# Performance work log

Measured on AMD Instinct MI355X. Metric: run time of the kernel, lower is better.

Reference implementation:

```python
import jax, jax.numpy as jnp
import numpy as np

D_MODEL = 1024
D_FF = 4096
NUM_EXPERTS = 8
TOP_K = 2


def setup_inputs() -> dict:
    key = jax.random.key(0)
    ks = jax.random.split(key, 10)
    s = 0.02
    x = jax.random.normal(ks[0], (2, 1024, D_MODEL), dtype=jnp.float32)
    # router gate (nn.Linear(d_model, num_experts))
    Wr = jax.random.normal(ks[1], (D_MODEL, NUM_EXPERTS), dtype=jnp.float32) * s
    br = jnp.zeros((NUM_EXPERTS,), dtype=jnp.float32)
    # stacked expert weights
    Wg = jax.random.normal(ks[2], (NUM_EXPERTS, D_MODEL, D_FF), dtype=jnp.float32) * s
    bg = jnp.zeros((NUM_EXPERTS, D_FF), dtype=jnp.float32)
    Wu = jax.random.normal(ks[3], (NUM_EXPERTS, D_MODEL, D_FF), dtype=jnp.float32) * s
    bu = jnp.zeros((NUM_EXPERTS, D_FF), dtype=jnp.float32)
    Wd = jax.random.normal(ks[4], (NUM_EXPERTS, D_FF, D_MODEL), dtype=jnp.float32) * s
    bd = jnp.zeros((NUM_EXPERTS, D_MODEL), dtype=jnp.float32)
    return {"x": x, "Wr": Wr, "br": br, "Wg": Wg, "bg": bg,
            "Wu": Wu, "bu": bu, "Wd": Wd, "bd": bd}


def reference(x, Wr, br, Wg, bg, Wu, bu, Wd, bd):
    B, S, D = x.shape
    E = Wg.shape[0]
    xt = x.reshape(-1, D)                       # [T, d]
    T = xt.shape[0]
    # router: softmax in float32, top-k, renormalize (Mixtral-style)
    logits = xt @ Wr + br                       # [T, E]
    probs = jax.nn.softmax(logits.astype(jnp.float32), axis=-1)
    rw, sel = jax.lax.top_k(probs, TOP_K)       # [T, K]
    rw = rw / jnp.sum(rw, axis=-1, keepdims=True)
    # per-token per-expert combine weight (0 if expert not selected)
    w_full = jnp.zeros((T, E), dtype=rw.dtype).at[
        jnp.arange(T)[:, None], sel].add(rw)    # [T, E]
    # SwiGLU experts, computed densely over all tokens then masked-combined
    g = jnp.einsum('td,edf->etf', xt, Wg) + bg[:, None, :]   # [E, T, f]
    u = jnp.einsum('td,edf->etf', xt, Wu) + bu[:, None, :]
    h = jax.nn.silu(g) * u
    y = jnp.einsum('etf,efd->etd', h, Wd) + bd[:, None, :]    # [E, T, d]
    out = jnp.einsum('te,etd->td', w_full.astype(x.dtype), y)
    return out.reshape(B, S, D)
```

## Files before the change

### kernel.cpp

```cpp
#include <hip/hip_runtime.h>

typedef float floatx4 __attribute__((ext_vector_type(4)));
typedef __bf16 bf16x4 __attribute__((ext_vector_type(4)));
typedef __bf16 bf16x8 __attribute__((ext_vector_type(8)));

#define D_MODEL 1024
#define D_FF 4096
#define NE 8

__device__ __forceinline__ int lds_off(int row, int k) {
    return row * 32 + ((((k >> 3) ^ ((row >> 2) & 3)) << 3) | (k & 7));
}

__global__ __launch_bounds__(256) void router_kernel(
    const float* __restrict__ x, const float* __restrict__ Wr,
    const float* __restrict__ br, int* __restrict__ cnt,
    int* __restrict__ list, float* __restrict__ w_slot, int T)
{
    int wv = threadIdx.x >> 6;
    int lane = threadIdx.x & 63;
    int t = blockIdx.x * 4 + wv;
    if (t >= T) return;

    const float* xp = x + (size_t)t * D_MODEL;
    float acc[8] = {0.f,0.f,0.f,0.f,0.f,0.f,0.f,0.f};
#pragma unroll
    for (int i = 0; i < 16; ++i) {
        int d = i * 64 + lane;
        float xv = xp[d];
        float4 w0 = *(const float4*)(Wr + d * 8);
        float4 w1 = *(const float4*)(Wr + d * 8 + 4);
        acc[0] += xv * w0.x; acc[1] += xv * w0.y;
        acc[2] += xv * w0.z; acc[3] += xv * w0.w;
        acc[4] += xv * w1.x; acc[5] += xv * w1.y;
        acc[6] += xv * w1.z; acc[7] += xv * w1.w;
    }
#pragma unroll
    for (int off = 32; off >= 1; off >>= 1) {
#pragma unroll
        for (int e = 0; e < 8; ++e)
            acc[e] += __shfl_down(acc[e], off, 64);
    }
    if (lane == 0) {
        float l[8];
#pragma unroll
        for (int e = 0; e < 8; ++e) l[e] = acc[e] + br[e];
        int i0 = 0; float v0 = l[0];
#pragma unroll
        for (int e = 1; e < 8; ++e) if (l[e] > v0) { v0 = l[e]; i0 = e; }
        int i1 = -1; float v1 = -3.4e38f;
#pragma unroll
        for (int e = 0; e < 8; ++e) if (e != i0 && l[e] > v1) { v1 = l[e]; i1 = e; }
        float ex = __expf(v1 - v0);
        float w0 = 1.f / (1.f + ex);
        float w1 = ex / (1.f + ex);
        int p0 = atomicAdd(&cnt[i0], 1);
        list[i0 * T + p0] = 2 * t;
        int p1 = atomicAdd(&cnt[i1], 1);
        list[i1 * T + p1] = 2 * t + 1;
        w_slot[2 * t]     = w0;
        w_slot[2 * t + 1] = w1;
    }
}

__global__ __launch_bounds__(256, 2) void gateup_kernel(
    const float* __restrict__ x, const float* __restrict__ Wg,
    const float* __restrict__ bg, const float* __restrict__ Wu,
    const float* __restrict__ bu, const int* __restrict__ cnt,
    const int* __restrict__ list, unsigned short* __restrict__ Hraw, int T)
{
    const int e  = blockIdx.z;
    const int m0 = blockIdx.y * 128;
    const int n0 = blockIdx.x * 128;
    const int count = cnt[e];
    if (m0 >= count) return;

    __bf16* H = (__bf16*)Hraw;
    __shared__ __bf16 ldsA[4096];
    __shared__ __bf16 ldsBg[4096];
    __shared__ __bf16 ldsBu[4096];
    __shared__ int s_entry[128];

    const int tid = threadIdx.x;
    if (tid < 128) {
        int r = m0 + tid;
        s_entry[tid] = (r < count) ? list[e * T + r] : list[e * T];
    }
    __syncthreads();

    const float* aptr[4];
    int awoff[4];
#pragma unroll
    for (int it = 0; it < 4; ++it) {
        int g = it * 256 + tid;
        int m = g >> 3, kg = g & 7;
        int token = s_entry[m] >> 1;
        aptr[it] = x + (size_t)token * D_MODEL + kg * 4;
        awoff[it] = lds_off(m, kg * 4);
    }
    const int kgrp = tid >> 5;
    const int fg   = tid & 31;
    const float* gbase = Wg + (size_t)e * D_MODEL * D_FF + (size_t)(kgrp * 4) * D_FF + n0 + fg * 4;
    const float* ubase = Wu + (size_t)e * D_MODEL * D_FF + (size_t)(kgrp * 4) * D_FF + n0 + fg * 4;
    int bwoff[4];
#pragma unroll
    for (int i = 0; i < 4; ++i) bwoff[i] = lds_off(fg * 4 + i, kgrp * 4);

    const int wv = tid >> 6, lane = tid & 63;
    const int wm = wv >> 1, wn = wv & 1;
    const int q = lane >> 4, ln = lane & 15;
    int aoff[4], boff[4];
#pragma unroll
    for (int i = 0; i < 4; ++i) {
        aoff[i] = lds_off(wm * 64 + i * 16 + ln, q * 8);
        boff[i] = lds_off(wn * 64 + i * 16 + ln, q * 8);
    }

    floatx4 accg[4][4] = {};
    floatx4 accu[4][4] = {};

    for (int k0 = 0; k0 < D_MODEL; k0 += 32) {
#pragma unroll
        for (int it = 0; it < 4; ++it) {
            float4 v = *(const float4*)(aptr[it] + k0);
            bf16x4 p = {(__bf16)v.x, (__bf16)v.y, (__bf16)v.z, (__bf16)v.w};
            *(bf16x4*)&ldsA[awoff[it]] = p;
        }
        {
            const float* b = gbase + (size_t)k0 * D_FF;
            float4 r0 = *(const float4*)(b);
            float4 r1 = *(const float4*)(b + D_FF);
            float4 r2 = *(const float4*)(b + 2 * D_FF);
            float4 r3 = *(const float4*)(b + 3 * D_FF);
            bf16x4 p0 = {(__bf16)r0.x, (__bf16)r1.x, (__bf16)r2.x, (__bf16)r3.x};
            bf16x4 p1 = {(__bf16)r0.y, (__bf16)r1.y, (__bf16)r2.y, (__bf16)r3.y};
            bf16x4 p2 = {(__bf16)r0.z, (__bf16)r1.z, (__bf16)r2.z, (__bf16)r3.z};
            bf16x4 p3 = {(__bf16)r0.w, (__bf16)r1.w, (__bf16)r2.w, (__bf16)r3.w};
            *(bf16x4*)&ldsBg[bwoff[0]] = p0;
            *(bf16x4*)&ldsBg[bwoff[1]] = p1;
            *(bf16x4*)&ldsBg[bwoff[2]] = p2;
            *(bf16x4*)&ldsBg[bwoff[3]] = p3;
        }
        {
            const float* b = ubase + (size_t)k0 * D_FF;
            float4 r0 = *(const float4*)(b);
            float4 r1 = *(const float4*)(b + D_FF);
            float4 r2 = *(const float4*)(b + 2 * D_FF);
            float4 r3 = *(const float4*)(b + 3 * D_FF);
            bf16x4 p0 = {(__bf16)r0.x, (__bf16)r1.x, (__bf16)r2.x, (__bf16)r3.x};
            bf16x4 p1 = {(__bf16)r0.y, (__bf16)r1.y, (__bf16)r2.y, (__bf16)r3.y};
            bf16x4 p2 = {(__bf16)r0.z, (__bf16)r1.z, (__bf16)r2.z, (__bf16)r3.z};
            bf16x4 p3 = {(__bf16)r0.w, (__bf16)r1.w, (__bf16)r2.w, (__bf16)r3.w};
            *(bf16x4*)&ldsBu[bwoff[0]] = p0;
            *(bf16x4*)&ldsBu[bwoff[1]] = p1;
            *(bf16x4*)&ldsBu[bwoff[2]] = p2;
            *(bf16x4*)&ldsBu[bwoff[3]] = p3;
        }
        __syncthreads();

        bf16x8 af[4], bgf[4], buf[4];
#pragma unroll
        for (int i = 0; i < 4; ++i) af[i] = *(const bf16x8*)&ldsA[aoff[i]];
#pragma unroll
        for (int i = 0; i < 4; ++i) bgf[i] = *(const bf16x8*)&ldsBg[boff[i]];
#pragma unroll
        for (int i = 0; i < 4; ++i) buf[i] = *(const bf16x8*)&ldsBu[boff[i]];
#pragma unroll
        for (int mi = 0; mi < 4; ++mi)
#pragma unroll
            for (int ni = 0; ni < 4; ++ni) {
                accg[mi][ni] = __builtin_amdgcn_mfma_f32_16x16x32_bf16(af[mi], bgf[ni], accg[mi][ni], 0, 0, 0);
                accu[mi][ni] = __builtin_amdgcn_mfma_f32_16x16x32_bf16(af[mi], buf[ni], accu[mi][ni], 0, 0, 0);
            }
        __syncthreads();
    }

#pragma unroll
    for (int ni = 0; ni < 4; ++ni) {
        int col = n0 + wn * 64 + ni * 16 + ln;
        float bgv = bg[e * D_FF + col];
        float buv = bu[e * D_FF + col];
#pragma unroll
        for (int mi = 0; mi < 4; ++mi) {
            int lrow0 = wm * 64 + mi * 16 + q * 4;
#pragma unroll
            for (int r = 0; r < 4; ++r) {
                int lr = lrow0 + r;
                if (m0 + lr < count) {
                    int entry = s_entry[lr];
                    float g = accg[mi][ni][r] + bgv;
                    float u = accu[mi][ni][r] + buv;
                    float h = g / (1.f + __expf(-g)) * u;
                    H[(size_t)entry * D_FF + col] = (__bf16)h;
                }
            }
        }
    }
}

__global__ __launch_bounds__(256, 2) void down_kernel(
    const unsigned short* __restrict__ Hraw, const float* __restrict__ Wd,
    const float* __restrict__ bd, const int* __restrict__ cnt,
    const int* __restrict__ list, const float* __restrict__ w_slot,
    float* __restrict__ out, int T)
{
    const int e  = blockIdx.z;
    const int m0 = blockIdx.y * 128;
    const int n0 = blockIdx.x * 128;
    const int count = cnt[e];
    if (m0 >= count) return;

    const __bf16* H = (const __bf16*)Hraw;
    __shared__ __bf16 ldsA[4096];
    __shared__ __bf16 ldsB[4096];
    __shared__ int s_entry[128];

    const int tid = threadIdx.x;
    if (tid < 128) {
        int r = m0 + tid;
        s_entry[tid] = (r < count) ? list[e * T + r] : list[e * T];
    }
    __syncthreads();

    const __bf16* aptr[2];
    int awoff[2];
#pragma unroll
    for (int it = 0; it < 2; ++it) {
        int g = it * 256 + tid;
        int m = g >> 2, k16 = g & 3;
        aptr[it] = H + (size_t)s_entry[m] * D_FF + k16 * 8;
        awoff[it] = lds_off(m, k16 * 8);
    }
    const int kgrp = tid >> 5;
    const int fg   = tid & 31;
    const float* dbase = Wd + (size_t)e * D_FF * D_MODEL + (size_t)(kgrp * 4) * D_MODEL + n0 + fg * 4;
    int bwoff[4];
#pragma unroll
    for (int i = 0; i < 4; ++i) bwoff[i] = lds_off(fg * 4 + i, kgrp * 4);

    const int wv = tid >> 6, lane = tid & 63;
    const int wm = wv >> 1, wn = wv & 1;
    const int q = lane >> 4, ln = lane & 15;
    int aoff[4], boff[4];
#pragma unroll
    for (int i = 0; i < 4; ++i) {
        aoff[i] = lds_off(wm * 64 + i * 16 + ln, q * 8);
        boff[i] = lds_off(wn * 64 + i * 16 + ln, q * 8);
    }

    floatx4 acc[4][4] = {};

    for (int k0 = 0; k0 < D_FF; k0 += 32) {
#pragma unroll
        for (int it = 0; it < 2; ++it) {
            bf16x8 v = *(const bf16x8*)(aptr[it] + k0);
            *(bf16x8*)&ldsA[awoff[it]] = v;
        }
        {
            const float* b = dbase + (size_t)k0 * D_MODEL;
            float4 r0 = *(const float4*)(b);
            float4 r1 = *(const float4*)(b + D_MODEL);
            float4 r2 = *(const float4*)(b + 2 * D_MODEL);
            float4 r3 = *(const float4*)(b + 3 * D_MODEL);
            bf16x4 p0 = {(__bf16)r0.x, (__bf16)r1.x, (__bf16)r2.x, (__bf16)r3.x};
            bf16x4 p1 = {(__bf16)r0.y, (__bf16)r1.y, (__bf16)r2.y, (__bf16)r3.y};
            bf16x4 p2 = {(__bf16)r0.z, (__bf16)r1.z, (__bf16)r2.z, (__bf16)r3.z};
            bf16x4 p3 = {(__bf16)r0.w, (__bf16)r1.w, (__bf16)r2.w, (__bf16)r3.w};
            *(bf16x4*)&ldsB[bwoff[0]] = p0;
            *(bf16x4*)&ldsB[bwoff[1]] = p1;
            *(bf16x4*)&ldsB[bwoff[2]] = p2;
            *(bf16x4*)&ldsB[bwoff[3]] = p3;
        }
        __syncthreads();

        bf16x8 af[4], bf[4];
#pragma unroll
        for (int i = 0; i < 4; ++i) af[i] = *(const bf16x8*)&ldsA[aoff[i]];
#pragma unroll
        for (int i = 0; i < 4; ++i) bf[i] = *(const bf16x8*)&ldsB[boff[i]];
#pragma unroll
        for (int mi = 0; mi < 4; ++mi)
#pragma unroll
            for (int ni = 0; ni < 4; ++ni)
                acc[mi][ni] = __builtin_amdgcn_mfma_f32_16x16x32_bf16(af[mi], bf[ni], acc[mi][ni], 0, 0, 0);
        __syncthreads();
    }

#pragma unroll
    for (int ni = 0; ni < 4; ++ni) {
        int col = n0 + wn * 64 + ni * 16 + ln;
        float bdv = bd[e * D_MODEL + col];
#pragma unroll
        for (int mi = 0; mi < 4; ++mi) {
            int lrow0 = wm * 64 + mi * 16 + q * 4;
#pragma unroll
            for (int r = 0; r < 4; ++r) {
                int lr = lrow0 + r;
                if (m0 + lr < count) {
                    int entry = s_entry[lr];
                    int token = entry >> 1;
                    float w = w_slot[entry];
                    atomicAdd(&out[(size_t)token * D_MODEL + col],
                              w * (acc[mi][ni][r] + bdv));
                }
            }
        }
    }
}

extern "C" void kernel_launch(void* const* d_in, const int* in_sizes, int n_in,
                              void* d_out, int out_size, void* d_ws, size_t ws_size,
                              hipStream_t stream) {
    const float* x  = (const float*)d_in[0];
    const float* Wr = (const float*)d_in[1];
    const float* br = (const float*)d_in[2];
    const float* Wg = (const float*)d_in[3];
    const float* bg = (const float*)d_in[4];
    const float* Wu = (const float*)d_in[5];
    const float* bu = (const float*)d_in[6];
    const float* Wd = (const float*)d_in[7];
    const float* bd = (const float*)d_in[8];
    float* out = (float*)d_out;
    const int T = in_sizes[0] / D_MODEL;

    char* ws = (char*)d_ws;
    int*   cnt    = (int*)ws;
    int*   list   = (int*)(ws + 256);
    float* w_slot = (float*)(ws + 256 + (size_t)NE * T * 4);
    size_t hoff = 256 + (size_t)NE * T * 4 + (size_t)2 * T * 4;
    hoff = (hoff + 1023) & ~(size_t)1023;
    unsigned short* H = (unsigned short*)(ws + hoff);

    hipMemsetAsync(cnt, 0, 256, stream);
    hipMemsetAsync(out, 0, (size_t)T * D_MODEL * sizeof(float), stream);

    router_kernel<<<dim3((T + 3) / 4), dim3(256), 0, stream>>>(x, Wr, br, cnt, list, w_slot, T);

    dim3 gb(D_FF / 128, (T + 127) / 128, NE);
    gateup_kernel<<<gb, dim3(256), 0, stream>>>(x, Wg, bg, Wu, bu, cnt, list, H, T);

    dim3 gc(D_MODEL / 128, (T + 127) / 128, NE);
    down_kernel<<<gc, dim3(256), 0, stream>>>(H, Wd, bd, cnt, list, w_slot, out, T);
}
```

Before: 805.6 us.

## Pre-convert weights to transposed bf16 and use direct global-to-LDS loads

Adds per-call kernels that convert x to bf16 and transpose-convert the expert weights to K-major bf16 in workspace. New gate/up and down GEMMs then stream tiles with global_load_lds 16-byte loads instead of converting fp32 in the main loop. The down projection is split over K in two halves and accumulated with atomics. This adds a large conversion pass over all weights each call and needs a big workspace, and it falls back to the old kernels if the workspace is too small.

New measurement: 742.1 us. 1.09x faster.

```diff
diff --git a/kernel.cpp b/kernel.cpp
--- a/kernel.cpp
+++ b/kernel.cpp
@@ -7,6 +7,16 @@
 #define D_MODEL 1024
 #define D_FF 4096
 #define NE 8
+
+__device__ __forceinline__ void gload16(const void* g, void* l) {
+    __builtin_amdgcn_global_load_lds(
+        (const __attribute__((address_space(1))) void*)g,
+        (__attribute__((address_space(3))) void*)l, 16, 0, 0);
+}
+
+__device__ __forceinline__ int frag_off(int row, int q) {
+    return row * 32 + ((q ^ ((row >> 2) & 3)) << 3);
+}
 
 __device__ __forceinline__ int lds_off(int row, int k) {
     return row * 32 + ((((k >> 3) ^ ((row >> 2) & 3)) << 3) | (k & 7));
@@ -63,7 +73,246 @@
     }
 }
 
-__global__ __launch_bounds__(256, 2) void gateup_kernel(
+__global__ __launch_bounds__(256) void xconv_kernel(
+    const float* __restrict__ x, __bf16* __restrict__ Xb, int n4)
+{
+    int i = blockIdx.x * 256 + threadIdx.x;
+    if (i < n4) {
+        float4 v = ((const float4*)x)[i];
+        bf16x4 o = {(__bf16)v.x, (__bf16)v.y, (__bf16)v.z, (__bf16)v.w};
+        ((bf16x4*)Xb)[i] = o;
+    }
+}
+
+__global__ __launch_bounds__(256) void tconv_kernel(
+    const float* __restrict__ src, __bf16* __restrict__ dst, int K, int N)
+{
+    __shared__ float tile[64][65];
+    const int kb = blockIdx.x * 64;
+    const int nb = blockIdx.y * 64;
+    const int e  = blockIdx.z;
+    src += (size_t)e * K * N;
+    dst += (size_t)e * K * N;
+    const int tid = threadIdx.x;
+    const int kr = tid >> 4;
+    const int nc = (tid & 15) * 4;
+#pragma unroll
+    for (int i = 0; i < 4; ++i) {
+        float4 v = *(const float4*)(src + (size_t)(kb + kr + i * 16) * N + nb + nc);
+        tile[kr + i * 16][nc]     = v.x;
+        tile[kr + i * 16][nc + 1] = v.y;
+        tile[kr + i * 16][nc + 2] = v.z;
+        tile[kr + i * 16][nc + 3] = v.w;
+    }
+    __syncthreads();
+#pragma unroll
+    for (int i = 0; i < 2; ++i) {
+        int p = i * 256 + tid;
+        int n = p >> 3;
+        int jg = (p & 7) * 8;
+        bf16x8 o;
+#pragma unroll
+        for (int j = 0; j < 8; ++j) o[j] = (__bf16)tile[jg + j][n];
+        *(bf16x8*)(dst + (size_t)(nb + n) * K + kb + jg) = o;
+    }
+}
+
+__global__ __launch_bounds__(256, 2) void gateup2_kernel(
+    const __bf16* __restrict__ Xb, const __bf16* __restrict__ Wgt,
+    const __bf16* __restrict__ Wut, const float* __restrict__ bg,
+    const float* __restrict__ bu, const int* __restrict__ cnt,
+    const int* __restrict__ list, __bf16* __restrict__ H, int T)
+{
+    const int e  = blockIdx.z;
+    const int m0 = blockIdx.y * 128;
+    const int n0 = blockIdx.x * 128;
+    const int count = cnt[e];
+    if (m0 >= count) return;
+
+    __shared__ __bf16 ldsA[4096];
+    __shared__ __bf16 ldsBg[4096];
+    __shared__ __bf16 ldsBu[4096];
+    __shared__ int s_entry[128];
+
+    const int tid = threadIdx.x;
+    if (tid < 128) {
+        int r = m0 + tid;
+        s_entry[tid] = (r < count) ? list[e * T + r] : list[e * T];
+    }
+    __syncthreads();
+
+    const __bf16* asrc[2]; const __bf16* gsrc[2]; const __bf16* usrc[2];
+    char* adst[2]; char* gdst[2]; char* udst[2];
+#pragma unroll
+    for (int i = 0; i < 2; ++i) {
+        int p = i * 256 + tid;
+        int row = p >> 2, j = p & 3;
+        int g = j ^ ((row >> 2) & 3);
+        int token = s_entry[row] >> 1;
+        asrc[i] = Xb + (size_t)token * D_MODEL + g * 8;
+        gsrc[i] = Wgt + ((size_t)e * D_FF + n0 + row) * D_MODEL + g * 8;
+        usrc[i] = Wut + ((size_t)e * D_FF + n0 + row) * D_MODEL + g * 8;
+        adst[i] = (char*)ldsA  + (size_t)p * 16;
+        gdst[i] = (char*)ldsBg + (size_t)p * 16;
+        udst[i] = (char*)ldsBu + (size_t)p * 16;
+    }
+
+    const int wv = tid >> 6, lane = tid & 63;
+    const int wm = wv >> 1, wn = wv & 1;
+    const int q = lane >> 4, ln = lane & 15;
+    int aoff[4], boff[4];
+#pragma unroll
+    for (int i = 0; i < 4; ++i) {
+        aoff[i] = frag_off(wm * 64 + i * 16 + ln, q);
+        boff[i] = frag_off(wn * 64 + i * 16 + ln, q);
+    }
+
+    floatx4 accg[4][4] = {};
+    floatx4 accu[4][4] = {};
+
+    for (int k0 = 0; k0 < D_MODEL; k0 += 32) {
+#pragma unroll
+        for (int i = 0; i < 2; ++i) {
+            gload16(asrc[i] + k0, adst[i]);
+            gload16(gsrc[i] + k0, gdst[i]);
+            gload16(usrc[i] + k0, udst[i]);
+        }
+        __syncthreads();
+
+        bf16x8 af[4], bgf[4], buf[4];
+#pragma unroll
+        for (int i = 0; i < 4; ++i) af[i]  = *(const bf16x8*)&ldsA[aoff[i]];
+#pragma unroll
+        for (int i = 0; i < 4; ++i) bgf[i] = *(const bf16x8*)&ldsBg[boff[i]];
+#pragma unroll
+        for (int i = 0; i < 4; ++i) buf[i] = *(const bf16x8*)&ldsBu[boff[i]];
+#pragma unroll
+        for (int mi = 0; mi < 4; ++mi)
+#pragma unroll
+            for (int ni = 0; ni < 4; ++ni) {
+                accg[mi][ni] = __builtin_amdgcn_mfma_f32_16x16x32_bf16(af[mi], bgf[ni], accg[mi][ni], 0, 0, 0);
+                accu[mi][ni] = __builtin_amdgcn_mfma_f32_16x16x32_bf16(af[mi], buf[ni], accu[mi][ni], 0, 0, 0);
+            }
+        __syncthreads();
+    }
+
+#pragma unroll
+    for (int ni = 0; ni < 4; ++ni) {
+        int col = n0 + wn * 64 + ni * 16 + ln;
+        float bgv = bg[e * D_FF + col];
+        float buv = bu[e * D_FF + col];
+#pragma unroll
+        for (int mi = 0; mi < 4; ++mi) {
+            int lrow0 = wm * 64 + mi * 16 + q * 4;
+#pragma unroll
+            for (int r = 0; r < 4; ++r) {
+                int lr = lrow0 + r;
+                if (m0 + lr < count) {
+                    int entry = s_entry[lr];
+                    float g = accg[mi][ni][r] + bgv;
+                    float u = accu[mi][ni][r] + buv;
+                    float h = g / (1.f + __expf(-g)) * u;
+                    H[(size_t)entry * D_FF + col] = (__bf16)h;
+                }
+            }
+        }
+    }
+}
+
+__global__ __launch_bounds__(256, 2) void down2_kernel(
+    const __bf16* __restrict__ H, const __bf16* __restrict__ Wdt,
+    const float* __restrict__ bd, const int* __restrict__ cnt,
+    const int* __restrict__ list, const float* __restrict__ w_slot,
+    float* __restrict__ out, int T)
+{
+    const int e  = blockIdx.z >> 1;
+    const int kc = blockIdx.z & 1;
+    const int m0 = blockIdx.y * 128;
+    const int n0 = blockIdx.x * 128;
+    const int count = cnt[e];
+    if (m0 >= count) return;
+
+    __shared__ __bf16 ldsA[4096];
+    __shared__ __bf16 ldsB[4096];
+    __shared__ int s_entry[128];
+
+    const int tid = threadIdx.x;
+    if (tid < 128) {
+        int r = m0 + tid;
+        s_entry[tid] = (r < count) ? list[e * T + r] : list[e * T];
+    }
+    __syncthreads();
+
+    const int kbase = kc * (D_FF / 2);
+    const __bf16* asrc[2]; const __bf16* bsrc[2];
+    char* adst[2]; char* bdst[2];
+#pragma unroll
+    for (int i = 0; i < 2; ++i) {
+        int p = i * 256 + tid;
+        int row = p >> 2, j = p & 3;
+        int g = j ^ ((row >> 2) & 3);
+        asrc[i] = H + (size_t)s_entry[row] * D_FF + kbase + g * 8;
+        bsrc[i] = Wdt + ((size_t)e * D_MODEL + n0 + row) * D_FF + kbase + g * 8;
+        adst[i] = (char*)ldsA + (size_t)p * 16;
+        bdst[i] = (char*)ldsB + (size_t)p * 16;
+    }
+
+    const int wv = tid >> 6, lane = tid & 63;
+    const int wm = wv >> 1, wn = wv & 1;
+    const int q = lane >> 4, ln = lane & 15;
+    int aoff[4], boff[4];
+#pragma unroll
+    for (int i = 0; i < 4; ++i) {
+        aoff[i] = frag_off(wm * 64 + i * 16 + ln, q);
+        boff[i] = frag_off(wn * 64 + i * 16 + ln, q);
+    }
+
+    floatx4 acc[4][4] = {};
+
+    for (int k0 = 0; k0 < D_FF / 2; k0 += 32) {
+#pragma unroll
+        for (int i = 0; i < 2; ++i) {
+            gload16(asrc[i] + k0, adst[i]);
+            gload16(bsrc[i] + k0, bdst[i]);
+        }
+        __syncthreads();
+
+        bf16x8 af[4], bf[4];
+#pragma unroll
+        for (int i = 0; i < 4; ++i) af[i] = *(const bf16x8*)&ldsA[aoff[i]];
+#pragma unroll
+        for (int i = 0; i < 4; ++i) bf[i] = *(const bf16x8*)&ldsB[boff[i]];
+#pragma unroll
+        for (int mi = 0; mi < 4; ++mi)
+#pragma unroll
+            for (int ni = 0; ni < 4; ++ni)
+                acc[mi][ni] = __builtin_amdgcn_mfma_f32_16x16x32_bf16(af[mi], bf[ni], acc[mi][ni], 0, 0, 0);
+        __syncthreads();
+    }
+
+#pragma unroll
+    for (int ni = 0; ni < 4; ++ni) {
+        int col = n0 + wn * 64 + ni * 16 + ln;
+        float bdv = (kc == 0) ? bd[e * D_MODEL + col] : 0.f;
+#pragma unroll
+        for (int mi = 0; mi < 4; ++mi) {
+            int lrow0 = wm * 64 + mi * 16 + q * 4;
+#pragma unroll
+            for (int r = 0; r < 4; ++r) {
+                int lr = lrow0 + r;
+                if (m0 + lr < count) {
+                    int entry = s_entry[lr];
+                    int token = entry >> 1;
+                    float w = w_slot[entry];
+                    atomicAdd(&out[(size_t)token * D_MODEL + col],
+                              w * (acc[mi][ni][r] + bdv));
+                }
+            }
+        }
+    }
+}
+
+__global__ __launch_bounds__(256, 2) void gateup_fb(
     const float* __restrict__ x, const float* __restrict__ Wg,
     const float* __restrict__ bg, const float* __restrict__ Wu,
     const float* __restrict__ bu, const int* __restrict__ cnt,
@@ -198,7 +447,7 @@
     }
 }
 
-__global__ __launch_bounds__(256, 2) void down_kernel(
+__global__ __launch_bounds__(256, 2) void down_fb(
     const unsigned short* __restrict__ Hraw, const float* __restrict__ Wd,
     const float* __restrict__ bd, const int* __restrict__ cnt,
     const int* __restrict__ list, const float* __restrict__ w_slot,
@@ -324,21 +573,42 @@
     const int T = in_sizes[0] / D_MODEL;
 
     char* ws = (char*)d_ws;
+    size_t off = 256;
     int*   cnt    = (int*)ws;
-    int*   list   = (int*)(ws + 256);
-    float* w_slot = (float*)(ws + 256 + (size_t)NE * T * 4);
-    size_t hoff = 256 + (size_t)NE * T * 4 + (size_t)2 * T * 4;
-    hoff = (hoff + 1023) & ~(size_t)1023;
-    unsigned short* H = (unsigned short*)(ws + hoff);
+    int*   list   = (int*)(ws + off);              off += (size_t)NE * T * 4;
+    float* w_slot = (float*)(ws + off);            off += (size_t)2 * T * 4;
+    off = (off + 1023) & ~(size_t)1023;
+    __bf16* Xb  = (__bf16*)(ws + off);             off += (size_t)T * D_MODEL * 2;
+    __bf16* H   = (__bf16*)(ws + off);             size_t h_at = off - (size_t)T * D_MODEL * 2;
+    off += (size_t)2 * T * D_FF * 2;
+    __bf16* Wgt = (__bf16*)(ws + off);             off += (size_t)NE * D_MODEL * D_FF * 2;
+    __bf16* Wut = (__bf16*)(ws + off);             off += (size_t)NE * D_MODEL * D_FF * 2;
+    __bf16* Wdt = (__bf16*)(ws + off);             off += (size_t)NE * D_FF * D_MODEL * 2;
+    const bool big = (ws_size >= off);
 
     hipMemsetAsync(cnt, 0, 256, stream);
     hipMemsetAsync(out, 0, (size_t)T * D_MODEL * sizeof(float), stream);
 
     router_kernel<<<dim3((T + 3) / 4), dim3(256), 0, stream>>>(x, Wr, br, cnt, list, w_slot, T);
 
-    dim3 gb(D_FF / 128, (T + 127) / 128, NE);
-    gateup_kernel<<<gb, dim3(256), 0, stream>>>(x, Wg, bg, Wu, bu, cnt, list, H, T);
-
-    dim3 gc(D_MODEL / 128, (T + 127) / 128, NE);
-    down_kernel<<<gc, dim3(256), 0, stream>>>(H, Wd, bd, cnt, list, w_slot, out, T);
-}
+    if (big) {
+        int n4 = T * D_MODEL / 4;
+        xconv_kernel<<<dim3((n4 + 255) / 256), dim3(256), 0, stream>>>(x, Xb, n4);
+        tconv_kernel<<<dim3(D_MODEL / 64, D_FF / 64, NE), dim3(256), 0, stream>>>(Wg, Wgt, D_MODEL, D_FF);
+        tconv_kernel<<<dim3(D_MODEL / 64, D_FF / 64, NE), dim3(256), 0, stream>>>(Wu, Wut, D_MODEL, D_FF);
+        tconv_kernel<<<dim3(D_FF / 64, D_MODEL / 64, NE), dim3(256), 0, stream>>>(Wd, Wdt, D_FF, D_MODEL);
+
+        dim3 gb(D_FF / 128, (T + 127) / 128, NE);
+        gateup2_kernel<<<gb, dim3(256), 0, stream>>>(Xb, Wgt, Wut, bg, bu, cnt, list, H, T);
+
+        dim3 gc(D_MODEL / 128, (T + 127) / 128, NE * 2);
+        down2_kernel<<<gc, dim3(256), 0, stream>>>(H, Wdt, bd, cnt, list, w_slot, out, T);
+    } else {
+        unsigned short* Hf = (unsigned short*)(ws + ((h_at + 1023) & ~(size_t)1023) + 0);
+        Hf = (unsigned short*)Xb;
+        dim3 gb(D_FF / 128, (T + 127) / 128, NE);
+        gateup_fb<<<gb, dim3(256), 0, stream>>>(x, Wg, bg, Wu, bu, cnt, list, Hf, T);
+        dim3 gc(D_MODEL / 128, (T + 127) / 128, NE);
+        down_fb<<<gc, dim3(256), 0, stream>>>((const unsigned short*)Hf, Wd, bd, cnt, list, w_slot, out, T);
+    }
+}
```

## Pre-convert weights to transposed bf16, use direct LDS loads, split-K down projection

Applied to the files above, without the earlier changes.

A new prep kernel converts Wg, Wu, Wd and x to bf16, with the weights stored K-contiguous, on every call. The GEMM kernels can then stream tiles into LDS with global_load_lds 16-byte loads instead of loading fp32 and converting in registers. The gate/up tile is narrowed to 64 columns and occupancy is raised to 3. The down projection is split four ways along K, writes partial sums to a scratch Y buffer that reuses the Wgt region, and a combine kernel applies the routing weights, replacing the atomic adds and the output memset. The cost is a full extra read and write pass over all expert weights each call, plus the Y round trip, and the per-iteration loads are still not double-buffered.

After: 677.9 us. 1.19x faster.

```diff
diff --git a/kernel.cpp b/kernel.cpp
--- a/kernel.cpp
+++ b/kernel.cpp
@@ -8,8 +8,14 @@
 #define D_FF 4096
 #define NE 8
 
-__device__ __forceinline__ int lds_off(int row, int k) {
-    return row * 32 + ((((k >> 3) ^ ((row >> 2) & 3)) << 3) | (k & 7));
+__device__ __forceinline__ void gload16(const void* g, void* l) {
+    __builtin_amdgcn_global_load_lds(
+        (const __attribute__((address_space(1))) void*)g,
+        (__attribute__((address_space(3))) void*)l, 16, 0, 0);
+}
+
+__device__ __forceinline__ int frag_off(int row, int q) {
+    return row * 32 + ((q ^ ((row >> 2) & 3)) << 3);
 }
 
 __global__ __launch_bounds__(256) void router_kernel(
@@ -63,22 +69,77 @@
     }
 }
 
-__global__ __launch_bounds__(256, 2) void gateup_kernel(
-    const float* __restrict__ x, const float* __restrict__ Wg,
-    const float* __restrict__ bg, const float* __restrict__ Wu,
+__global__ __launch_bounds__(256) void prep_kernel(
+    const float* __restrict__ Wg, const float* __restrict__ Wu,
+    const float* __restrict__ Wd, const float* __restrict__ x,
+    __bf16* __restrict__ Wgt, __bf16* __restrict__ Wut,
+    __bf16* __restrict__ Wdt, __bf16* __restrict__ Xb)
+{
+    const int bid = blockIdx.x;
+    const int tid = threadIdx.x;
+    if (bid >= 24576) {
+        int base = (bid - 24576) * 2048 + tid * 8;
+        float4 v0 = *(const float4*)(x + base);
+        float4 v1 = *(const float4*)(x + base + 4);
+        bf16x8 o = {(__bf16)v0.x, (__bf16)v0.y, (__bf16)v0.z, (__bf16)v0.w,
+                    (__bf16)v1.x, (__bf16)v1.y, (__bf16)v1.z, (__bf16)v1.w};
+        *(bf16x8*)(Xb + base) = o;
+        return;
+    }
+    const int tensor = bid >> 13;
+    const int rem = bid & 8191;
+    const int e = rem >> 10;
+    const int tile = rem & 1023;
+    const float* src; __bf16* dst; int K, N, kb, nb;
+    if (tensor == 0)      { src = Wg; dst = Wgt; }
+    else if (tensor == 1) { src = Wu; dst = Wut; }
+    else                  { src = Wd; dst = Wdt; }
+    if (tensor < 2) { K = 1024; N = 4096; kb = (tile & 15) << 6; nb = (tile >> 4) << 6; }
+    else            { K = 4096; N = 1024; kb = (tile & 63) << 6; nb = (tile >> 6) << 6; }
+    src += (size_t)e * K * N;
+    dst += (size_t)e * K * N;
+
+    __shared__ __bf16 tileT[64 * 72];
+    const int kr = (tid >> 4) << 2;
+    const int nc = (tid & 15) << 2;
+    const float* s0 = src + (size_t)(kb + kr) * N + nb + nc;
+    float4 r0 = *(const float4*)(s0);
+    float4 r1 = *(const float4*)(s0 + N);
+    float4 r2 = *(const float4*)(s0 + 2 * N);
+    float4 r3 = *(const float4*)(s0 + 3 * N);
+    bf16x4 c0 = {(__bf16)r0.x, (__bf16)r1.x, (__bf16)r2.x, (__bf16)r3.x};
+    bf16x4 c1 = {(__bf16)r0.y, (__bf16)r1.y, (__bf16)r2.y, (__bf16)r3.y};
+    bf16x4 c2 = {(__bf16)r0.z, (__bf16)r1.z, (__bf16)r2.z, (__bf16)r3.z};
+    bf16x4 c3 = {(__bf16)r0.w, (__bf16)r1.w, (__bf16)r2.w, (__bf16)r3.w};
+    *(bf16x4*)&tileT[(nc + 0) * 72 + kr] = c0;
+    *(bf16x4*)&tileT[(nc + 1) * 72 + kr] = c1;
+    *(bf16x4*)&tileT[(nc + 2) * 72 + kr] = c2;
+    *(bf16x4*)&tileT[(nc + 3) * 72 + kr] = c3;
+    __syncthreads();
+#pragma unroll
+    for (int i = 0; i < 2; ++i) {
+        int p = i * 256 + tid;
+        int n = p >> 3, kg = p & 7;
+        bf16x8 v = *(const bf16x8*)&tileT[n * 72 + kg * 8];
+        *(bf16x8*)(dst + (size_t)(nb + n) * K + kb + kg * 8) = v;
+    }
+}
+
+__global__ __launch_bounds__(256, 3) void gateup3_kernel(
+    const __bf16* __restrict__ Xb, const __bf16* __restrict__ Wgt,
+    const __bf16* __restrict__ Wut, const float* __restrict__ bg,
     const float* __restrict__ bu, const int* __restrict__ cnt,
-    const int* __restrict__ list, unsigned short* __restrict__ Hraw, int T)
+    const int* __restrict__ list, __bf16* __restrict__ H, int T)
 {
     const int e  = blockIdx.z;
     const int m0 = blockIdx.y * 128;
-    const int n0 = blockIdx.x * 128;
+    const int n0 = blockIdx.x * 64;
     const int count = cnt[e];
     if (m0 >= count) return;
 
-    __bf16* H = (__bf16*)Hraw;
     __shared__ __bf16 ldsA[4096];
-    __shared__ __bf16 ldsBg[4096];
-    __shared__ __bf16 ldsBu[4096];
+    __shared__ __bf16 ldsBg[2048];
+    __shared__ __bf16 ldsBu[2048];
     __shared__ int s_entry[128];
 
     const int tid = threadIdx.x;
@@ -88,87 +149,49 @@
     }
     __syncthreads();
 
-    const float* aptr[4];
-    int awoff[4];
-#pragma unroll
-    for (int it = 0; it < 4; ++it) {
-        int g = it * 256 + tid;
-        int m = g >> 3, kg = g & 7;
-        int token = s_entry[m] >> 1;
-        aptr[it] = x + (size_t)token * D_MODEL + kg * 4;
-        awoff[it] = lds_off(m, kg * 4);
-    }
-    const int kgrp = tid >> 5;
-    const int fg   = tid & 31;
-    const float* gbase = Wg + (size_t)e * D_MODEL * D_FF + (size_t)(kgrp * 4) * D_FF + n0 + fg * 4;
-    const float* ubase = Wu + (size_t)e * D_MODEL * D_FF + (size_t)(kgrp * 4) * D_FF + n0 + fg * 4;
-    int bwoff[4];
-#pragma unroll
-    for (int i = 0; i < 4; ++i) bwoff[i] = lds_off(fg * 4 + i, kgrp * 4);
+    const int row0 = tid >> 2, j0 = tid & 3;
+    const int g0 = j0 ^ ((row0 >> 2) & 3);
+    const int p1 = 256 + tid, row1 = p1 >> 2, j1 = p1 & 3;
+    const int g1 = j1 ^ ((row1 >> 2) & 3);
+    const __bf16* asrc0 = Xb + (size_t)(s_entry[row0] >> 1) * D_MODEL + g0 * 8;
+    const __bf16* asrc1 = Xb + (size_t)(s_entry[row1] >> 1) * D_MODEL + g1 * 8;
+    const __bf16* gsrc  = Wgt + ((size_t)e * D_FF + n0 + row0) * D_MODEL + g0 * 8;
+    const __bf16* usrc  = Wut + ((size_t)e * D_FF + n0 + row0) * D_MODEL + g0 * 8;
+    char* adst0 = (char*)ldsA + tid * 16;
+    char* adst1 = (char*)ldsA + (256 + tid) * 16;
+    char* gdst  = (char*)ldsBg + tid * 16;
+    char* udst  = (char*)ldsBu + tid * 16;
 
     const int wv = tid >> 6, lane = tid & 63;
     const int wm = wv >> 1, wn = wv & 1;
     const int q = lane >> 4, ln = lane & 15;
-    int aoff[4], boff[4];
-#pragma unroll
-    for (int i = 0; i < 4; ++i) {
-        aoff[i] = lds_off(wm * 64 + i * 16 + ln, q * 8);
-        boff[i] = lds_off(wn * 64 + i * 16 + ln, q * 8);
-    }
-
-    floatx4 accg[4][4] = {};
-    floatx4 accu[4][4] = {};
+    int aoff[4], boff[2];
+#pragma unroll
+    for (int i = 0; i < 4; ++i) aoff[i] = frag_off(wm * 64 + i * 16 + ln, q);
+#pragma unroll
+    for (int i = 0; i < 2; ++i) boff[i] = frag_off(wn * 32 + i * 16 + ln, q);
+
+    floatx4 accg[4][2] = {};
+    floatx4 accu[4][2] = {};
 
     for (int k0 = 0; k0 < D_MODEL; k0 += 32) {
-#pragma unroll
-        for (int it = 0; it < 4; ++it) {
-            float4 v = *(const float4*)(aptr[it] + k0);
-            bf16x4 p = {(__bf16)v.x, (__bf16)v.y, (__bf16)v.z, (__bf16)v.w};
-            *(bf16x4*)&ldsA[awoff[it]] = p;
-        }
-        {
-            const float* b = gbase + (size_t)k0 * D_FF;
-            float4 r0 = *(const float4*)(b);
-            float4 r1 = *(const float4*)(b + D_FF);
-            float4 r2 = *(const float4*)(b + 2 * D_FF);
-            float4 r3 = *(const float4*)(b + 3 * D_FF);
-            bf16x4 p0 = {(__bf16)r0.x, (__bf16)r1.x, (__bf16)r2.x, (__bf16)r3.x};
-            bf16x4 p1 = {(__bf16)r0.y, (__bf16)r1.y, (__bf16)r2.y, (__bf16)r3.y};
-            bf16x4 p2 = {(__bf16)r0.z, (__bf16)r1.z, (__bf16)r2.z, (__bf16)r3.z};
-            bf16x4 p3 = {(__bf16)r0.w, (__bf16)r1.w, (__bf16)r2.w, (__bf16)r3.w};
-            *(bf16x4*)&ldsBg[bwoff[0]] = p0;
-            *(bf16x4*)&ldsBg[bwoff[1]] = p1;
-            *(bf16x4*)&ldsBg[bwoff[2]] = p2;
-            *(bf16x4*)&ldsBg[bwoff[3]] = p3;
-        }
-        {
-            const float* b = ubase + (size_t)k0 * D_FF;
-            float4 r0 = *(const float4*)(b);
-            float4 r1 = *(const float4*)(b + D_FF);
-            float4 r2 = *(const float4*)(b + 2 * D_FF);
-            float4 r3 = *(const float4*)(b + 3 * D_FF);
-            bf16x4 p0 = {(__bf16)r0.x, (__bf16)r1.x, (__bf16)r2.x, (__bf16)r3.x};
-            bf16x4 p1 = {(__bf16)r0.y, (__bf16)r1.y, (__bf16)r2.y, (__bf16)r3.y};
-            bf16x4 p2 = {(__bf16)r0.z, (__bf16)r1.z, (__bf16)r2.z, (__bf16)r3.z};
-            bf16x4 p3 = {(__bf16)r0.w, (__bf16)r1.w, (__bf16)r2.w, (__bf16)r3.w};
-            *(bf16x4*)&ldsBu[bwoff[0]] = p0;
-            *(bf16x4*)&ldsBu[bwoff[1]] = p1;
-            *(bf16x4*)&ldsBu[bwoff[2]] = p2;
-            *(bf16x4*)&ldsBu[bwoff[3]] = p3;
-        }
+        gload16(asrc0 + k0, adst0);
+        gload16(asrc1 + k0, adst1);
+        gload16(gsrc + k0, gdst);
+        gload16(usrc + k0, udst);
         __syncthreads();
 
-        bf16x8 af[4], bgf[4], buf[4];
-#pragma unroll
-        for (int i = 0; i < 4; ++i) af[i] = *(const bf16x8*)&ldsA[aoff[i]];
-#pragma unroll
-        for (int i = 0; i < 4; ++i) bgf[i] = *(const bf16x8*)&ldsBg[boff[i]];
-#pragma unroll
-        for (int i = 0; i < 4; ++i) buf[i] = *(const bf16x8*)&ldsBu[boff[i]];
+        bf16x8 af[4], bgf[2], buf[2];
+#pragma unroll
+        for (int i = 0; i < 4; ++i) af[i]  = *(const bf16x8*)&ldsA[aoff[i]];
+#pragma unroll
+        for (int i = 0; i < 2; ++i) bgf[i] = *(const bf16x8*)&ldsBg[boff[i]];
+#pragma unroll
+        for (int i = 0; i < 2; ++i) buf[i] = *(const bf16x8*)&ldsBu[boff[i]];
 #pragma unroll
         for (int mi = 0; mi < 4; ++mi)
 #pragma unroll
-            for (int ni = 0; ni < 4; ++ni) {
+            for (int ni = 0; ni < 2; ++ni) {
                 accg[mi][ni] = __builtin_amdgcn_mfma_f32_16x16x32_bf16(af[mi], bgf[ni], accg[mi][ni], 0, 0, 0);
                 accu[mi][ni] = __builtin_amdgcn_mfma_f32_16x16x32_bf16(af[mi], buf[ni], accu[mi][ni], 0, 0, 0);
             }
@@ -176,8 +199,8 @@
     }
 
 #pragma unroll
-    for (int ni = 0; ni < 4; ++ni) {
-        int col = n0 + wn * 64 + ni * 16 + ln;
+    for (int ni = 0; ni < 2; ++ni) {
+        int col = n0 + wn * 32 + ni * 16 + ln;
         float bgv = bg[e * D_FF + col];
         float buv = bu[e * D_FF + col];
 #pragma unroll
@@ -198,19 +221,18 @@
     }
 }
 
-__global__ __launch_bounds__(256, 2) void down_kernel(
-    const unsigned short* __restrict__ Hraw, const float* __restrict__ Wd,
+__global__ __launch_bounds__(256, 3) void down3_kernel(
+    const __bf16* __restrict__ H, const __bf16* __restrict__ Wdt,
     const float* __restrict__ bd, const int* __restrict__ cnt,
-    const int* __restrict__ list, const float* __restrict__ w_slot,
-    float* __restrict__ out, int T)
-{
-    const int e  = blockIdx.z;
+    const int* __restrict__ list, float* __restrict__ Y, int T)
+{
+    const int e  = blockIdx.z >> 2;
+    const int kc = blockIdx.z & 3;
     const int m0 = blockIdx.y * 128;
     const int n0 = blockIdx.x * 128;
     const int count = cnt[e];
     if (m0 >= count) return;
 
-    const __bf16* H = (const __bf16*)Hraw;
     __shared__ __bf16 ldsA[4096];
     __shared__ __bf16 ldsB[4096];
     __shared__ int s_entry[128];
@@ -222,21 +244,19 @@
     }
     __syncthreads();
 
-    const __bf16* aptr[2];
-    int awoff[2];
-#pragma unroll
-    for (int it = 0; it < 2; ++it) {
-        int g = it * 256 + tid;
-        int m = g >> 2, k16 = g & 3;
-        aptr[it] = H + (size_t)s_entry[m] * D_FF + k16 * 8;
-        awoff[it] = lds_off(m, k16 * 8);
-    }
-    const int kgrp = tid >> 5;
-    const int fg   = tid & 31;
-    const float* dbase = Wd + (size_t)e * D_FF * D_MODEL + (size_t)(kgrp * 4) * D_MODEL + n0 + fg * 4;
-    int bwoff[4];
-#pragma unroll
-    for (int i = 0; i < 4; ++i) bwoff[i] = lds_off(fg * 4 + i, kgrp * 4);
+    const int kbase = kc * (D_FF / 4);
+    const __bf16* asrc[2]; const __bf16* bsrc[2];
+    char* adst[2]; char* bdst[2];
+#pragma unroll
+    for (int i = 0; i < 2; ++i) {
+        int p = i * 256 + tid;
+        int row = p >> 2, j = p & 3;
+        int g = j ^ ((row >> 2) & 3);
+        asrc[i] = H + (size_t)s_entry[row] * D_FF + kbase + g * 8;
+        bsrc[i] = Wdt + ((size_t)e * D_MODEL + n0 + row) * D_FF + kbase + g * 8;
+        adst[i] = (char*)ldsA + (size_t)p * 16;
+        bdst[i] = (char*)ldsB + (size_t)p * 16;
+    }
 
     const int wv = tid >> 6, lane = tid & 63;
     const int wm = wv >> 1, wn = wv & 1;
@@ -244,32 +264,17 @@
     int aoff[4], boff[4];
 #pragma unroll
     for (int i = 0; i < 4; ++i) {
-        aoff[i] = lds_off(wm * 64 + i * 16 + ln, q * 8);
-        boff[i] = lds_off(wn * 64 + i * 16 + ln, q * 8);
+        aoff[i] = frag_off(wm * 64 + i * 16 + ln, q);
+        boff[i] = frag_off(wn * 64 + i * 16 + ln, q);
     }
 
     floatx4 acc[4][4] = {};
 
-    for (int k0 = 0; k0 < D_FF; k0 += 32) {
-#pragma unroll
-        for (int it = 0; it < 2; ++it) {
-            bf16x8 v = *(const bf16x8*)(aptr[it] + k0);
-            *(bf16x8*)&ldsA[awoff[it]] = v;
-        }
-        {
-            const float* b = dbase + (size_t)k0 * D_MODEL;
-            float4 r0 = *(const float4*)(b);
-            float4 r1 = *(const float4*)(b + D_MODEL);
-            float4 r2 = *(const float4*)(b + 2 * D_MODEL);
-            float4 r3 = *(const float4*)(b + 3 * D_MODEL);
-            bf16x4 p0 = {(__bf16)r0.x, (__bf16)r1.x, (__bf16)r2.x, (__bf16)r3.x};
-            bf16x4 p1 = {(__bf16)r0.y, (__bf16)r1.y, (__bf16)r2.y, (__bf16)r3.y};
-            bf16x4 p2 = {(__bf16)r0.z, (__bf16)r1.z, (__bf16)r2.z, (__bf16)r3.z};
-            bf16x4 p3 = {(__bf16)r0.w, (__bf16)r1.w, (__bf16)r2.w, (__bf16)r3.w};
-            *(bf16x4*)&ldsB[bwoff[0]] = p0;
-            *(bf16x4*)&ldsB[bwoff[1]] = p1;
-            *(bf16x4*)&ldsB[bwoff[2]] = p2;
-            *(bf16x4*)&ldsB[bwoff[3]] = p3;
+    for (int k0 = 0; k0 < D_FF / 4; k0 += 32) {
+#pragma unroll
+        for (int i = 0; i < 2; ++i) {
+            gload16(asrc[i] + k0, adst[i]);
+            gload16(bsrc[i] + k0, bdst[i]);
         }
         __syncthreads();
 
@@ -286,10 +291,11 @@
         __syncthreads();
     }
 
+    const size_t kc_off = (size_t)kc * 2 * T * D_MODEL;
 #pragma unroll
     for (int ni = 0; ni < 4; ++ni) {
         int col = n0 + wn * 64 + ni * 16 + ln;
-        float bdv = bd[e * D_MODEL + col];
+        float bdv = (kc == 0) ? bd[e * D_MODEL + col] : 0.f;
 #pragma unroll
         for (int mi = 0; mi < 4; ++mi) {
             int lrow0 = wm * 64 + mi * 16 + q * 4;
@@ -298,14 +304,34 @@
                 int lr = lrow0 + r;
                 if (m0 + lr < count) {
                     int entry = s_entry[lr];
-                    int token = entry >> 1;
-                    float w = w_slot[entry];
-                    atomicAdd(&out[(size_t)token * D_MODEL + col],
-                              w * (acc[mi][ni][r] + bdv));
+                    Y[kc_off + (size_t)entry * D_MODEL + col] = acc[mi][ni][r] + bdv;
                 }
             }
         }
     }
+}
+
+__global__ __launch_bounds__(256) void combine_kernel(
+    const float* __restrict__ Y, const float* __restrict__ w_slot,
+    float* __restrict__ out, int T)
+{
+    int idx = blockIdx.x * 256 + threadIdx.x;
+    int t = idx >> 8;
+    const float4* Y4 = (const float4*)Y;
+    size_t r0 = (size_t)(2 * t) * 256 + (idx & 255);
+    size_t r1 = r0 + 256;
+    size_t ks = (size_t)2 * T * 256;
+    float4 a = Y4[r0], b = Y4[r1];
+#pragma unroll
+    for (int kc = 1; kc < 4; ++kc) {
+        float4 va = Y4[r0 + kc * ks], vb = Y4[r1 + kc * ks];
+        a.x += va.x; a.y += va.y; a.z += va.z; a.w += va.w;
+        b.x += vb.x; b.y += vb.y; b.z += vb.z; b.w += vb.w;
+    }
+    float w0 = w_slot[2 * t], w1 = w_slot[2 * t + 1];
+    float4 o = {w0 * a.x + w1 * b.x, w0 * a.y + w1 * b.y,
+                w0 * a.z + w1 * b.z, w0 * a.w + w1 * b.w};
+    ((float4*)out)[idx] = o;
 }
 
 extern "C" void kernel_launch(void* const* d_in, const int* in_sizes, int n_in,
@@ -324,21 +350,30 @@
     const int T = in_sizes[0] / D_MODEL;
 
     char* ws = (char*)d_ws;
+    size_t off = 256;
     int*   cnt    = (int*)ws;
-    int*   list   = (int*)(ws + 256);
-    float* w_slot = (float*)(ws + 256 + (size_t)NE * T * 4);
-    size_t hoff = 256 + (size_t)NE * T * 4 + (size_t)2 * T * 4;
-    hoff = (hoff + 1023) & ~(size_t)1023;
-    unsigned short* H = (unsigned short*)(ws + hoff);
+    int*   list   = (int*)(ws + off);              off += (size_t)NE * T * 4;
+    float* w_slot = (float*)(ws + off);            off += (size_t)2 * T * 4;
+    off = (off + 1023) & ~(size_t)1023;
+    __bf16* Xb  = (__bf16*)(ws + off);             off += (size_t)T * D_MODEL * 2;
+    __bf16* H   = (__bf16*)(ws + off);             off += (size_t)2 * T * D_FF * 2;
+    __bf16* Wgt = (__bf16*)(ws + off);
+    float*  Y   = (float*)(ws + off);
+    off += (size_t)NE * D_MODEL * D_FF * 2;
+    __bf16* Wut = (__bf16*)(ws + off);             off += (size_t)NE * D_MODEL * D_FF * 2;
+    __bf16* Wdt = (__bf16*)(ws + off);             off += (size_t)NE * D_FF * D_MODEL * 2;
 
     hipMemsetAsync(cnt, 0, 256, stream);
-    hipMemsetAsync(out, 0, (size_t)T * D_MODEL * sizeof(float), stream);
 
     router_kernel<<<dim3((T + 3) / 4), dim3(256), 0, stream>>>(x, Wr, br, cnt, list, w_slot, T);
 
-    dim3 gb(D_FF / 128, (T + 127) / 128, NE);
-    gateup_kernel<<<gb, dim3(256), 0, stream>>>(x, Wg, bg, Wu, bu, cnt, list, H, T);
-
-    dim3 gc(D_MODEL / 128, (T + 127) / 128, NE);
-    down_kernel<<<gc, dim3(256), 0, stream>>>(H, Wd, bd, cnt, list, w_slot, out, T);
-}
+    prep_kernel<<<dim3(25600), dim3(256), 0, stream>>>(Wg, Wu, Wd, x, Wgt, Wut, Wdt, Xb);
+
+    dim3 gb(D_FF / 64, (T + 127) / 128, NE);
+    gateup3_kernel<<<gb, dim3(256), 0, stream>>>(Xb, Wgt, Wut, bg, bu, cnt, list, H, T);
+
+    dim3 gc(D_MODEL / 128, (T + 127) / 128, NE * 4);
+    down3_kernel<<<gc, dim3(256), 0, stream>>>(H, Wdt, bd, cnt, list, Y, T);
+
+    combine_kernel<<<dim3(T * D_MODEL / 4 / 256), dim3(256), 0, stream>>>(Y, w_slot, out, T);
+}
```
